# Kernel optimization log

Measured on AMD Instinct MI355X. Metric: run time of the kernel, lower is better.

The kernel has to match this reference:

```python
import jax, jax.numpy as jnp
import numpy as np

IN_F = 2048
OUT_F = 2048
N_ROWS = 8192


def _perm(n):
    # t_o(n) is a permutation matrix P with P[i, p(i)] = 1, p(i) = (4i mod n) + (4i // n)
    i = np.arange(n)
    return (4 * i) % n + (4 * i) // n


def _inv(p):
    inv = np.empty_like(p)
    inv[p] = np.arange(len(p))
    return inv

# (P_in^T @ H)[a, :] = H[i, :] where p_in(i) = a  ->  rows indexed by inv(p_in)
_INV_P_IN = _inv(_perm(IN_F))
# (H @ P_out)[:, b] = H[:, j] where p_out(j) = b  ->  cols indexed by inv(p_out)
_INV_P_OUT = _inv(_perm(OUT_F))


def make_quaternion_mul(kernel):
    # kernel: (in//4, out); split along dim 1 into quaternion components
    r, i, j, k = jnp.split(kernel, 4, axis=1)
    r2 = jnp.concatenate([r, -i, -j, -k], axis=1)
    i2 = jnp.concatenate([i, r, -k, j], axis=1)
    j2 = jnp.concatenate([j, k, r, -i], axis=1)
    k2 = jnp.concatenate([k, -j, i, r], axis=1)
    return jnp.concatenate([r2, i2, j2, k2], axis=0)  # (in, out)


def setup_inputs() -> dict:
    key = jax.random.key(0)
    k1, k2, k3 = jax.random.split(key, 3)
    inp = jax.random.normal(k1, (N_ROWS, IN_F), dtype=jnp.float32)
    weight = jax.random.normal(k2, (IN_F // 4, OUT_F), dtype=jnp.float32) * (1.0 / np.sqrt(IN_F // 4))
    bias = jax.random.normal(k3, (OUT_F,), dtype=jnp.float32) * 0.01
    return {"input": inp, "weight": weight, "bias": bias}


def reference(input, weight, bias):
    hamilton = make_quaternion_mul(weight)                 # (in, out)
    # swap=True: hamilton = L^T @ hamilton @ R, both pure permutations
    hamilton = hamilton[_INV_P_IN][:, _INV_P_OUT]
    support = input @ hamilton + bias[None, :]             # (N, out)
    return support
```

## Files before the change

kernel.cpp:

```cpp
#include <hip/hip_runtime.h>
#include <stdint.h>

#define IN_F 2048
#define OUT_F 2048
#define N_ROWS 8192

#define BM 256
#define BN 256
#define BK 32
#define NT (IN_F / BK)
#define TM_TILES (N_ROWS / BM)
#define TN_TILES (OUT_F / BN)
#define NWG (TM_TILES * TN_TILES)
#define TILE_SHORTS (BM * BK)
#define BUF_SHORTS (2 * TILE_SHORTS)

typedef __bf16 bf16x8 __attribute__((ext_vector_type(8)));
typedef float f32x4 __attribute__((ext_vector_type(4)));
typedef unsigned short ushortx8 __attribute__((ext_vector_type(8)));

__device__ __forceinline__ unsigned short f2bf(float f) {
  unsigned u = __builtin_bit_cast(unsigned, f);
  u += 0x7FFFu + ((u >> 16) & 1u);
  return (unsigned short)(u >> 16);
}

__device__ __forceinline__ void async16(void* lds, const void* g) {
  __builtin_amdgcn_global_load_lds(
      (const __attribute__((address_space(1))) void*)(uintptr_t)g,
      (__attribute__((address_space(3))) void*)(uint32_t)(uintptr_t)lds,
      16, 0, 0);
}

__device__ __forceinline__ bf16x8 ld8(const unsigned short* p) {
  return __builtin_bit_cast(bf16x8, *reinterpret_cast<const ushortx8*>(p));
}

__global__ __launch_bounds__(256) void k_prep(const float* __restrict__ A,
                                              unsigned short* __restrict__ AbT,
                                              const float* __restrict__ W,
                                              unsigned short* __restrict__ BtT) {
  const int bid = blockIdx.x;
  if (bid < 8192) {
    const int tile = bid >> 2;
    const int t = ((bid & 3) << 8) + threadIdx.x;
    const int r = t >> 2;
    const int ga = (t & 3) ^ ((r >> 1) & 3);
    const int R = tile >> 6, T = tile & 63;
    const float* src = A + (size_t)(R * 256 + r) * IN_F + T * 32 + ga * 8;
    const float4 v0 = *reinterpret_cast<const float4*>(src);
    const float4 v1 = *reinterpret_cast<const float4*>(src + 4);
    ushortx8 o;
    o[0] = f2bf(v0.x); o[1] = f2bf(v0.y); o[2] = f2bf(v0.z); o[3] = f2bf(v0.w);
    o[4] = f2bf(v1.x); o[5] = f2bf(v1.y); o[6] = f2bf(v1.z); o[7] = f2bf(v1.w);
    *reinterpret_cast<ushortx8*>(AbT + (size_t)tile * 8192 + t * 8) = o;
  } else {
    const int bb = bid - 8192;
    const int tile = bb >> 2;
    const int t = ((bb & 3) << 8) + threadIdx.x;
    const int r = t >> 2;
    const int ga = (t & 3) ^ ((r >> 1) & 3);
    const int Ct = tile >> 6, T = tile & 63;
    const int b = Ct * 256 + r;
    const int c = b & 3, v = b >> 2;
    const int a0 = T * 32 + ga * 8;
    ushortx8 o;
#pragma unroll
    for (int e = 0; e < 8; ++e) {
      const int a = a0 + e;
      const int q = a & 3, u = a >> 2;
      float w = W[(size_t)u * OUT_F + ((q ^ c) << 9) + v];
      if ((0x284E >> ((q << 2) | c)) & 1) w = -w;
      o[e] = f2bf(w);
    }
    *reinterpret_cast<ushortx8*>(BtT + (size_t)tile * 8192 + t * 8) = o;
  }
}

__global__ __launch_bounds__(512, 2) void k_gemm(const unsigned short* __restrict__ AbT,
                                                 const unsigned short* __restrict__ BtT,
                                                 const float* __restrict__ bias,
                                                 float* __restrict__ C) {
  __shared__ __align__(16) unsigned short lds[4 * BUF_SHORTS];

  const int tid = threadIdx.x;
  const int lane = tid & 63;
  const int w = tid >> 6;
  const int wm = w >> 2;
  const int wn = w & 3;
  const int fr = lane & 15;
  const int g = lane >> 4;

  const int wg = blockIdx.x;
  const int swz = (wg & 7) * (NWG >> 3) + (wg >> 3);
  const int tm = swz >> 3;
  const int tn = swz & 7;
  const int row0 = tm * BM, col0 = tn * BN;

  const unsigned short* baseA = AbT + (size_t)tm * 64 * 8192;
  const unsigned short* baseB = BtT + (size_t)tn * 64 * 8192;
  const int tOff0 = (w * 128 + lane) * 8;
  const int tOff1 = (w * 128 + 64 + lane) * 8;

#define STAGE(T)                                                   \
  do {                                                             \
    unsigned short* base_ = &lds[((T) & 3) * BUF_SHORTS];          \
    const unsigned short* sa_ = baseA + (size_t)(T) * 8192;        \
    const unsigned short* sb_ = baseB + (size_t)(T) * 8192;        \
    async16(base_ + tOff0, sa_ + tOff0);                           \
    async16(base_ + tOff1, sa_ + tOff1);                           \
    async16(base_ + TILE_SHORTS + tOff0, sb_ + tOff0);             \
    async16(base_ + TILE_SHORTS + tOff1, sb_ + tOff1);             \
  } while (0)

  int offA[8], offB[4];
#pragma unroll
  for (int m = 0; m < 8; ++m) {
    const int r = wm * 128 + m * 16 + fr;
    offA[m] = r * BK + ((g ^ ((r >> 1) & 3)) << 3);
  }
#pragma unroll
  for (int n = 0; n < 4; ++n) {
    const int r = wn * 64 + n * 16 + fr;
    offB[n] = TILE_SHORTS + r * BK + ((g ^ ((r >> 1) & 3)) << 3);
  }

  f32x4 acc[8][4] = {};
  bf16x8 bgE[4], bgO[4];

#define MFMA_(a_, b_, c_) __builtin_amdgcn_mfma_f32_16x16x32_bf16(a_, b_, c_, 0, 0, 0)

  STAGE(0);
  STAGE(1);
  STAGE(2);

#define STEP(T, BG_, VMSTR, DOSTAGE)                                          \
  do {                                                                        \
    asm volatile("s_waitcnt vmcnt(" VMSTR ")" ::: "memory");                  \
    __builtin_amdgcn_s_barrier();                                             \
    __builtin_amdgcn_sched_barrier(0);                                        \
    const unsigned short* b_ = &lds[((T) & 3) * BUF_SHORTS];                  \
    bf16x8 af[8];                                                             \
    _Pragma("unroll") for (int m = 0; m < 8; ++m) af[m] = ld8(b_ + offA[m]);  \
    _Pragma("unroll") for (int n = 0; n < 4; ++n) BG_[n] = ld8(b_ + offB[n]); \
    if (DOSTAGE) STAGE((T) + 3);                                              \
    __builtin_amdgcn_s_setprio(1);                                            \
    _Pragma("unroll") for (int m = 0; m < 8; ++m)                             \
      _Pragma("unroll") for (int n = 0; n < 4; ++n)                           \
        acc[m][n] = MFMA_(af[m], BG_[n], acc[m][n]);                          \
    __builtin_amdgcn_s_setprio(0);                                            \
  } while (0)

#pragma unroll 1
  for (int t = 0; t < NT - 4; t += 2) {
    STEP(t, bgE, "8", true);
    STEP(t + 1, bgO, "8", true);
  }
  STEP(NT - 4, bgE, "8", true);
  STEP(NT - 3, bgO, "8", false);
  STEP(NT - 2, bgE, "4", false);
  STEP(NT - 1, bgO, "0", false);

#undef STEP
#undef STAGE

  const int g4 = g << 2;
  float bv[4];
#pragma unroll
  for (int n = 0; n < 4; ++n) bv[n] = bias[col0 + wn * 64 + n * 16 + fr];
#pragma unroll
  for (int m = 0; m < 8; ++m) {
#pragma unroll
    for (int e = 0; e < 4; ++e) {
      const int row = row0 + wm * 128 + m * 16 + g4 + e;
      float* cp = C + (size_t)row * OUT_F + col0 + wn * 64 + fr;
#pragma unroll
      for (int n = 0; n < 4; ++n) cp[n * 16] = acc[m][n][e] + bv[n];
    }
  }
}

__global__ __launch_bounds__(256) void k_naive(const float* __restrict__ A,
                                               const float* __restrict__ W,
                                               const float* __restrict__ bias,
                                               float* __restrict__ C) {
  const int idx = blockIdx.x * 256 + threadIdx.x;
  const int m = idx >> 11;
  const int b = idx & (OUT_F - 1);
  const int c = b & 3, v = b >> 2;
  float acc = 0.f;
  const float* arow = A + (size_t)m * IN_F;
  for (int a = 0; a < IN_F; ++a) {
    const int q = a & 3, u = a >> 2;
    float h = W[(size_t)u * OUT_F + ((q ^ c) << 9) + v];
    if ((0x284E >> ((q << 2) | c)) & 1) h = -h;
    acc += arow[a] * h;
  }
  C[idx] = acc + bias[b];
}

extern "C" void kernel_launch(void* const* d_in, const int* in_sizes, int n_in,
                              void* d_out, int out_size, void* d_ws, size_t ws_size,
                              hipStream_t stream) {
  (void)in_sizes; (void)n_in; (void)out_size;
  const float* inp  = (const float*)d_in[0];
  const float* w    = (const float*)d_in[1];
  const float* bias = (const float*)d_in[2];
  float* out = (float*)d_out;

  const size_t needA = (size_t)N_ROWS * IN_F * sizeof(unsigned short);
  const size_t needB = (size_t)IN_F * OUT_F * sizeof(unsigned short);
  if (ws_size < needA + needB) {
    k_naive<<<(N_ROWS * OUT_F) / 256, 256, 0, stream>>>(inp, w, bias, out);
    return;
  }

  unsigned short* AbT = (unsigned short*)d_ws;
  unsigned short* BtT = AbT + (size_t)N_ROWS * IN_F;

  k_prep<<<8192 + 2048, 256, 0, stream>>>(inp, AbT, w, BtT);
  k_gemm<<<NWG, 512, 0, stream>>>(AbT, BtT, bias, out);
}
```

Baseline: 86.04 us.

## Process two K-tiles per barrier with a five-buffer LDS ring

The GEMM main loop now handles two BK tiles per synchronisation window instead of one. The LDS ring grows from four to five stage buffers, with explicit buffer indices arranged in a 10-tile rotation. Each window issues two prefetch stages between the fragment loads of its two tiles, which halves the number of s_barrier/waitcnt points and gives longer MFMA bursts. In exchange, LDS use rises to 160KB and live fragment registers roughly double, which may limit occupancy or scheduling.

```diff
diff --git a/kernel.cpp b/kernel.cpp
--- a/kernel.cpp
+++ b/kernel.cpp
@@ -81,7 +81,7 @@
                                                  const unsigned short* __restrict__ BtT,
                                                  const float* __restrict__ bias,
                                                  float* __restrict__ C) {
-  __shared__ __align__(16) unsigned short lds[4 * BUF_SHORTS];
+  __shared__ __align__(16) unsigned short lds[5 * BUF_SHORTS];
 
   const int tid = threadIdx.x;
   const int lane = tid & 63;
@@ -102,9 +102,9 @@
   const int tOff0 = (w * 128 + lane) * 8;
   const int tOff1 = (w * 128 + 64 + lane) * 8;
 
-#define STAGE(T)                                                   \
+#define STAGE(T, BUF)                                              \
   do {                                                             \
-    unsigned short* base_ = &lds[((T) & 3) * BUF_SHORTS];          \
+    unsigned short* base_ = &lds[(BUF) * BUF_SHORTS];              \
     const unsigned short* sa_ = baseA + (size_t)(T) * 8192;        \
     const unsigned short* sb_ = baseB + (size_t)(T) * 8192;        \
     async16(base_ + tOff0, sa_ + tOff0);                           \
@@ -126,42 +126,49 @@
   }
 
   f32x4 acc[8][4] = {};
-  bf16x8 bgE[4], bgO[4];
 
 #define MFMA_(a_, b_, c_) __builtin_amdgcn_mfma_f32_16x16x32_bf16(a_, b_, c_, 0, 0, 0)
 
-  STAGE(0);
-  STAGE(1);
-  STAGE(2);
-
-#define STEP(T, BG_, VMSTR, DOSTAGE)                                          \
+#define WINDOW(T, B0, B1, S0, S1, VMSTR, NS)                                  \
   do {                                                                        \
     asm volatile("s_waitcnt vmcnt(" VMSTR ")" ::: "memory");                  \
     __builtin_amdgcn_s_barrier();                                             \
     __builtin_amdgcn_sched_barrier(0);                                        \
-    const unsigned short* b_ = &lds[((T) & 3) * BUF_SHORTS];                  \
-    bf16x8 af[8];                                                             \
-    _Pragma("unroll") for (int m = 0; m < 8; ++m) af[m] = ld8(b_ + offA[m]);  \
-    _Pragma("unroll") for (int n = 0; n < 4; ++n) BG_[n] = ld8(b_ + offB[n]); \
-    if (DOSTAGE) STAGE((T) + 3);                                              \
+    const unsigned short* p0_ = &lds[(B0) * BUF_SHORTS];                      \
+    const unsigned short* p1_ = &lds[(B1) * BUF_SHORTS];                      \
+    bf16x8 bg0[4], bg1[4], af0[8], af1[8];                                    \
+    _Pragma("unroll") for (int n = 0; n < 4; ++n) bg0[n] = ld8(p0_ + offB[n]);\
+    _Pragma("unroll") for (int m = 0; m < 8; ++m) af0[m] = ld8(p0_ + offA[m]);\
+    if ((NS) >= 1) STAGE((T) + 3, S0);                                        \
+    if ((NS) >= 2) STAGE((T) + 4, S1);                                        \
+    _Pragma("unroll") for (int n = 0; n < 4; ++n) bg1[n] = ld8(p1_ + offB[n]);\
+    _Pragma("unroll") for (int m = 0; m < 8; ++m) af1[m] = ld8(p1_ + offA[m]);\
     __builtin_amdgcn_s_setprio(1);                                            \
     _Pragma("unroll") for (int m = 0; m < 8; ++m)                             \
       _Pragma("unroll") for (int n = 0; n < 4; ++n)                           \
-        acc[m][n] = MFMA_(af[m], BG_[n], acc[m][n]);                          \
+        acc[m][n] = MFMA_(af0[m], bg0[n], acc[m][n]);                         \
+    _Pragma("unroll") for (int m = 0; m < 8; ++m)                             \
+      _Pragma("unroll") for (int n = 0; n < 4; ++n)                           \
+        acc[m][n] = MFMA_(af1[m], bg1[n], acc[m][n]);                         \
     __builtin_amdgcn_s_setprio(0);                                            \
   } while (0)
 
+  STAGE(0, 0);
+  STAGE(1, 1);
+  STAGE(2, 2);
+
 #pragma unroll 1
-  for (int t = 0; t < NT - 4; t += 2) {
-    STEP(t, bgE, "8", true);
-    STEP(t + 1, bgO, "8", true);
-  }
-  STEP(NT - 4, bgE, "8", true);
-  STEP(NT - 3, bgO, "8", false);
-  STEP(NT - 2, bgE, "4", false);
-  STEP(NT - 1, bgO, "0", false);
-
-#undef STEP
+  for (int tb = 0; tb < NT - 4; tb += 10) {
+    WINDOW(tb + 0, 0, 1, 3, 4, "4", 2);
+    WINDOW(tb + 2, 2, 3, 0, 1, "4", 2);
+    WINDOW(tb + 4, 4, 0, 2, 3, "4", 2);
+    WINDOW(tb + 6, 1, 2, 4, 0, "4", 2);
+    WINDOW(tb + 8, 3, 4, 1, 2, "4", 2);
+  }
+  WINDOW(NT - 4, 0, 1, 3, 3, "4", 1);
+  WINDOW(NT - 2, 2, 3, 0, 0, "0", 0);
+
+#undef WINDOW
 #undef STAGE
 
   const int g4 = g << 2;
```

Result: slower. 93.60 us (+8.8%).
